# Optimization experiments

Measured on AMD Instinct MI355X. Metric: run time of the kernel, lower is better.

Reference implementation:

```python
import jax, jax.numpy as jnp
from jax import lax
import numpy as np


def _lap(cost):
    """Jonker-Volgenant shortest-augmenting-path LAP (same optimum as
    scipy.optimize.linear_sum_assignment) on cost [n, m] with n <= m.
    Returns for each row (0..n-1) the assigned column index."""
    n, m = cost.shape
    BIG = jnp.asarray(1e9, cost.dtype)
    a = jnp.pad(cost, ((1, 0), (1, 0)))  # 1-based rows/cols, [n+1, m+1]
    u = jnp.zeros(n + 1, cost.dtype)     # row duals
    v = jnp.zeros(m + 1, cost.dtype)     # col duals
    p = jnp.zeros(m + 1, jnp.int32)      # p[j] = row matched to col j (0 = free)

    def row_step(i, carry):
        u, v, p = carry
        p = p.at[0].set(i)  # virtual col 0 holds the row being inserted
        minv = jnp.full(m + 1, BIG, cost.dtype)
        used = jnp.zeros(m + 1, bool)
        way = jnp.zeros(m + 1, jnp.int32)

        def cond(s):
            u, v, p, way, minv, used, j0 = s
            return p[j0] != 0

        def body(s):
            u, v, p, way, minv, used, j0 = s
            used = used.at[j0].set(True)
            i0 = p[j0]
            cur = a[i0] - u[i0] - v                      # reduced costs, len m+1
            better = (cur < minv) & jnp.logical_not(used)
            minv = jnp.where(better, cur, minv)
            way = jnp.where(better, j0, way)
            masked = jnp.where(used, BIG, minv)
            j1 = jnp.argmin(masked).astype(jnp.int32)
            delta = masked[j1]
            u = u.at[p].add(jnp.where(used, delta, jnp.zeros((), cost.dtype)))
            v = jnp.where(used, v - delta, v)
            minv = jnp.where(used, minv, minv - delta)
            return (u, v, p, way, minv, used, j1)

        u, v, p, way, minv, used, j0 = lax.while_loop(
            cond, body, (u, v, p, way, minv, used, jnp.int32(0)))

        # backtrack the augmenting path
        def cond2(s):
            return s[1] != 0

        def body2(s):
            p, j0 = s
            j1 = way[j0]
            return (p.at[j0].set(p[j1]), j1)

        p, _ = lax.while_loop(cond2, body2, (p, j0))
        return (u, v, p)

    u, v, p = lax.fori_loop(1, n + 1, row_step, (u, v, p))
    # invert: row r (1-based) matched to col j  ->  ans[r-1] = j-1
    cols = jnp.arange(m + 1)
    valid = (p > 0) & (cols > 0)
    idx = jnp.where(valid, p - 1, n)  # invalid entries dumped into scratch slot n
    ans = jnp.zeros(n + 1, jnp.int32).at[idx].set((cols - 1).astype(jnp.int32))
    return ans[:n]


def _cdist_mm(x, y):
    """Batched euclidean cdist via the GEMM trick (torch use_mm_for_euclid_dist)."""
    x2 = jnp.sum(x * x, axis=-1)[..., :, None]   # [B, N, 1]
    y2 = jnp.sum(y * y, axis=-1)[..., None, :]   # [B, 1, M]
    xy = jnp.einsum('bnd,bmd->bnm', x, y)        # [B, N, M]
    return jnp.sqrt(jnp.maximum(x2 + y2 - 2.0 * xy, 0.0))


def setup_inputs() -> dict:
    key = jax.random.key(0)
    k1, k2 = jax.random.split(key)
    outputs = jax.random.normal(k1, (32, 512, 768), dtype=jnp.float32)
    targets = jax.random.normal(k2, (32, 200, 768), dtype=jnp.float32)
    return {"outputs": outputs, "targets": targets}


def reference(outputs, targets):
    # cost[b, n, m] = ||outputs[b, n] - targets[b, m]||_2  (block-diagonal slices
    # of the original cross-batch cdist are all that the matcher consumes)
    cost = _cdist_mm(outputs, targets)                       # [B, N, M]
    # solve with targets as rows (n=M <= m=N): pred column per gt row
    gt_to_pred = jax.vmap(_lap)(jnp.swapaxes(cost, 1, 2))    # [B, M]
    # scipy returns pred indices sorted ascending; replicate that ordering
    order = jnp.argsort(gt_to_pred, axis=1)                  # gt indices (index_j)
    index_i = jnp.take_along_axis(gt_to_pred, order, axis=1)
    index_j = order.astype(jnp.int32)
    return jnp.stack([index_i, index_j], axis=1)             # [B, 2, M] int32
```

## Files before the change

kernel.cpp:

```cpp
#include <hip/hip_runtime.h>
#include <math.h>

static constexpr int BATCH = 32;
static constexpr int NPRED = 512;
static constexpr int NTGT  = 200;
static constexpr int DIM   = 768;
#define BIGF  1e9f
#define USEDC 2e9f

__global__ __launch_bounds__(64) void row_norms_kernel(const float* __restrict__ x,
                                                       float* __restrict__ out) {
    int row = blockIdx.x;
    const float4* r = (const float4*)(x + (size_t)row * DIM);
    float s = 0.f;
#pragma unroll
    for (int k = 0; k < 3; ++k) {
        float4 v = r[threadIdx.x + 64 * k];
        s += v.x * v.x + v.y * v.y + v.z * v.z + v.w * v.w;
    }
#pragma unroll
    for (int off = 32; off; off >>= 1) s += __shfl_down(s, off);
    if (threadIdx.x == 0) out[row] = s;
}

__global__ __launch_bounds__(256) void cost_kernel(const float* __restrict__ O,
                                                   const float* __restrict__ T,
                                                   const float* __restrict__ no_arr,
                                                   const float* __restrict__ nt_arr,
                                                   float* __restrict__ cost) {
    const int b  = blockIdx.z;
    const int m0 = blockIdx.y * 32;
    const int n0 = blockIdx.x * 128;
    const float* Tb = T + (size_t)b * NTGT * DIM;
    const float* Ob = O + (size_t)b * NPRED * DIM;

    __shared__ float As[32][33];
    __shared__ float Bs[32][129];

    const int tid = threadIdx.x;
    const int tx = tid & 31;
    const int ty = tid >> 5;

    float acc[4][4] = {};

    for (int k0 = 0; k0 < DIM; k0 += 32) {
        {
            int ar = tid >> 3;
            int ak = (tid & 7) << 2;
            int gm = m0 + ar; if (gm > NTGT - 1) gm = NTGT - 1;
            float4 vA = *(const float4*)(Tb + (size_t)gm * DIM + k0 + ak);
            As[ak + 0][ar] = vA.x; As[ak + 1][ar] = vA.y;
            As[ak + 2][ar] = vA.z; As[ak + 3][ar] = vA.w;
        }
#pragma unroll
        for (int q = 0; q < 4; ++q) {
            int idx = q * 256 + tid;
            int br = idx >> 3;
            int bk = (idx & 7) << 2;
            float4 vB = *(const float4*)(Ob + (size_t)(n0 + br) * DIM + k0 + bk);
            Bs[bk + 0][br] = vB.x; Bs[bk + 1][br] = vB.y;
            Bs[bk + 2][br] = vB.z; Bs[bk + 3][br] = vB.w;
        }
        __syncthreads();
#pragma unroll
        for (int k = 0; k < 32; ++k) {
            float a0 = As[k][ty], a1 = As[k][ty + 8],
                  a2 = As[k][ty + 16], a3 = As[k][ty + 24];
            float b0 = Bs[k][tx],      b1 = Bs[k][tx + 32],
                  b2 = Bs[k][tx + 64], b3 = Bs[k][tx + 96];
            acc[0][0] += a0 * b0; acc[0][1] += a0 * b1; acc[0][2] += a0 * b2; acc[0][3] += a0 * b3;
            acc[1][0] += a1 * b0; acc[1][1] += a1 * b1; acc[1][2] += a1 * b2; acc[1][3] += a1 * b3;
            acc[2][0] += a2 * b0; acc[2][1] += a2 * b1; acc[2][2] += a2 * b2; acc[2][3] += a2 * b3;
            acc[3][0] += a3 * b0; acc[3][1] += a3 * b1; acc[3][2] += a3 * b2; acc[3][3] += a3 * b3;
        }
        __syncthreads();
    }

#pragma unroll
    for (int i = 0; i < 4; ++i) {
        int gm = m0 + ty + 8 * i;
        if (gm < NTGT) {
            float ntv = nt_arr[b * NTGT + gm];
#pragma unroll
            for (int j = 0; j < 4; ++j) {
                int gn = n0 + tx + 32 * j;
                float d2 = ntv + no_arr[b * NPRED + gn] - 2.0f * acc[i][j];
                cost[((size_t)b * NTGT + gm) * NPRED + gn] = sqrtf(fmaxf(d2, 0.0f));
            }
        }
    }
}

__device__ __forceinline__ int rl(int v, int l) {
    return __builtin_amdgcn_readlane(v, l);
}
__device__ __forceinline__ float rlf(float v, int l) {
    return __int_as_float(__builtin_amdgcn_readlane(__float_as_int(v), l));
}
__device__ __forceinline__ int sel8i(const int* a, int s) {
    int r = a[0];
#pragma unroll
    for (int k = 1; k < 8; ++k) r = (s == k) ? a[k] : r;
    return r;
}
__device__ __forceinline__ float sel8f(const float* a, int s) {
    float r = a[0];
#pragma unroll
    for (int k = 1; k < 8; ++k) r = (s == k) ? a[k] : r;
    return r;
}
__device__ __forceinline__ float dpp_min_f32(float x) {
    float t;
    t = __int_as_float(__builtin_amdgcn_update_dpp(__float_as_int(x), __float_as_int(x), 0x111, 0xF, 0xF, false)); x = fminf(x, t);
    t = __int_as_float(__builtin_amdgcn_update_dpp(__float_as_int(x), __float_as_int(x), 0x112, 0xF, 0xF, false)); x = fminf(x, t);
    t = __int_as_float(__builtin_amdgcn_update_dpp(__float_as_int(x), __float_as_int(x), 0x114, 0xF, 0xF, false)); x = fminf(x, t);
    t = __int_as_float(__builtin_amdgcn_update_dpp(__float_as_int(x), __float_as_int(x), 0x118, 0xF, 0xF, false)); x = fminf(x, t);
    t = __int_as_float(__builtin_amdgcn_update_dpp(__float_as_int(x), __float_as_int(x), 0x142, 0xF, 0xF, false)); x = fminf(x, t);
    t = __int_as_float(__builtin_amdgcn_update_dpp(__float_as_int(x), __float_as_int(x), 0x143, 0xF, 0xF, false)); x = fminf(x, t);
    return x;
}
__device__ __forceinline__ float tree8(const float* m, int& lq) {
    float v01 = (m[0] <= m[1]) ? m[0] : m[1];
    int   q01 = (m[0] <= m[1]) ? 0 : 1;
    float v23 = (m[2] <= m[3]) ? m[2] : m[3];
    int   q23 = (m[2] <= m[3]) ? 2 : 3;
    float v45 = (m[4] <= m[5]) ? m[4] : m[5];
    int   q45 = (m[4] <= m[5]) ? 4 : 5;
    float v67 = (m[6] <= m[7]) ? m[6] : m[7];
    int   q67 = (m[6] <= m[7]) ? 6 : 7;
    float v03 = (v01 <= v23) ? v01 : v23;
    int   q03 = (v01 <= v23) ? q01 : q23;
    float v47 = (v45 <= v67) ? v45 : v67;
    int   q47 = (v45 <= v67) ? q45 : q67;
    lq = (v03 <= v47) ? q03 : q47;
    return (v03 <= v47) ? v03 : v47;
}

__global__ __launch_bounds__(64) void lap_kernel(const float* __restrict__ cost,
                                                 int* __restrict__ out) {
    const int b = blockIdx.x;
    const int lane = threadIdx.x;
    const float* C = cost + (size_t)b * NTGT * NPRED;
    const float* Cl = C + lane * 8;

    __shared__ float u0[NTGT + 1];
    __shared__ int g2p[NTGT];

    for (int k = lane; k < NTGT + 1; k += 64) u0[k] = 0.f;

    float v[8], minv[8], up[8];
    int p_arr[8], way_arr[8];
#pragma unroll
    for (int q = 0; q < 8; ++q) {
        v[q] = 0.f; up[q] = 0.f; p_arr[q] = 0; way_arr[q] = 0;
    }
    __syncthreads();

    float4 ca = *(const float4*)(Cl);
    float4 cb = *(const float4*)(Cl + 4);
    float4 sa = ca, sb = cb;

    for (int i = 1; i <= NTGT; ++i) {
#pragma unroll
        for (int q = 0; q < 8; ++q) minv[q] = BIGF;
        float uI = 0.f;
        float u_i0 = 0.f;
        int j0 = 0;
        int j1 = 0;
        int spec_j = 0;

        for (int it = 0; it <= NPRED; ++it) {
            float c[8];
            c[0] = ca.x; c[1] = ca.y; c[2] = ca.z; c[3] = ca.w;
            c[4] = cb.x; c[5] = cb.y; c[6] = cb.z; c[7] = cb.w;

#pragma unroll
            for (int q = 0; q < 8; ++q) {
                float cur = (c[q] - u_i0) - v[q];
                bool usedq = (minv[q] == USEDC);
                float cure = usedq ? USEDC : cur;
                bool imp = cure < minv[q];
                minv[q] = imp ? cure : minv[q];
                way_arr[q] = imp ? j0 : way_arr[q];
            }

            int lq;
            float lval = tree8(minv, lq);
            int   psel = sel8i(p_arr, lq);
            float usel = sel8f(up, lq);
            float wmin = rlf(dpp_min_f32(lval), 63);
            unsigned long long mask = __ballot(lval == wmin);
            int w = (int)__builtin_ctzll(mask);
            int qw  = rl(lq, w);
            int i0n = rl(psel, w);
            float u_n = rlf(usel, w);
            float delta = wmin;
            j1 = w * 8 + qw + 1;
            bool done = (i0n == 0);

            if (!done) {
                if (j1 == spec_j) {
                    ca = sa; cb = sb;
                } else {
                    const float* Crow = Cl + (size_t)(i0n - 1) * NPRED;
                    ca = *(const float4*)(Crow);
                    cb = *(const float4*)(Crow + 4);
                }
            }

            uI += delta;
#pragma unroll
            for (int q = 0; q < 8; ++q) {
                bool usedq = (minv[q] == USEDC);
                v[q]    = usedq ? (v[q] - delta) : v[q];
                up[q]   = usedq ? (up[q] + delta) : up[q];
                minv[q] = usedq ? minv[q] : (minv[q] - delta);
            }
            int j1m1 = j1 - 1;
#pragma unroll
            for (int q = 0; q < 8; ++q) {
                bool mine = (lane * 8 + q) == j1m1;
                minv[q] = mine ? USEDC : minv[q];
            }

            if (done) break;

            {
                int lq2;
                float l2 = tree8(minv, lq2);
                int psel2 = sel8i(p_arr, lq2);
                float w2v = rlf(dpp_min_f32(l2), 63);
                unsigned long long m2 = __ballot(l2 == w2v);
                int w2 = (int)__builtin_ctzll(m2);
                int q2 = rl(lq2, w2);
                int p2 = rl(psel2, w2);
                int spec_new = w2 * 8 + q2 + 1;
                if (p2 != 0 && spec_new != spec_j) {
                    const float* Srow = Cl + (size_t)(p2 - 1) * NPRED;
                    sa = *(const float4*)(Srow);
                    sb = *(const float4*)(Srow + 4);
                }
                spec_j = spec_new;
            }

            u_i0 = u_n;
            j0 = j1;
        }

        if (i < NTGT) {
            const float* Crow = Cl + (size_t)i * NPRED;
            ca = *(const float4*)(Crow);
            cb = *(const float4*)(Crow + 4);
        }

#pragma unroll
        for (int q = 0; q < 8; ++q) {
            bool usedq = (minv[q] == USEDC);
            if (usedq && p_arr[q] != 0) u0[p_arr[q]] = up[q];
        }
        if (lane == 0) u0[i] = uI;

        {
            int j = j1;
            for (int s = 0; s <= NPRED; ++s) {
                int ow = (j - 1) >> 3, oq = (j - 1) & 7;
                int wj = rl(sel8i(way_arr, oq), ow);
                int pOfW;
                if (wj == 0) {
                    pOfW = i;
                } else {
                    int ow2 = (wj - 1) >> 3, oq2 = (wj - 1) & 7;
                    pOfW = rl(sel8i(p_arr, oq2), ow2);
                }
#pragma unroll
                for (int q = 0; q < 8; ++q) {
                    bool mine = (lane == ow) && (q == oq);
                    p_arr[q] = mine ? pOfW : p_arr[q];
                }
                if (wj == 0) break;
                j = wj;
            }
        }

        __syncthreads();
#pragma unroll
        for (int q = 0; q < 8; ++q) up[q] = u0[p_arr[q]];
    }

#pragma unroll
    for (int q = 0; q < 8; ++q) {
        int r = p_arr[q];
        if (r > 0) g2p[r - 1] = lane * 8 + q;
    }
    __syncthreads();

    for (int t = lane; t < NTGT; t += 64) {
        int myv = g2p[t];
        int rank = 0;
        for (int l = 0; l < NTGT; ++l) rank += (g2p[l] < myv) ? 1 : 0;
        out[b * 2 * NTGT + rank] = myv;
        out[b * 2 * NTGT + NTGT + rank] = t;
    }
}

extern "C" void kernel_launch(void* const* d_in, const int* in_sizes, int n_in,
                              void* d_out, int out_size, void* d_ws, size_t ws_size,
                              hipStream_t stream) {
    const float* outputs = (const float*)d_in[0];
    const float* targets = (const float*)d_in[1];
    int* out = (int*)d_out;

    float* cost   = (float*)d_ws;
    float* no_arr = cost + (size_t)BATCH * NTGT * NPRED;
    float* nt_arr = no_arr + (size_t)BATCH * NPRED;

    row_norms_kernel<<<BATCH * NPRED, 64, 0, stream>>>(outputs, no_arr);
    row_norms_kernel<<<BATCH * NTGT, 64, 0, stream>>>(targets, nt_arr);
    cost_kernel<<<dim3(NPRED / 128, (NTGT + 31) / 32, BATCH), 256, 0, stream>>>(
        outputs, targets, no_arr, nt_arr, cost);
    lap_kernel<<<BATCH, 64, 0, stream>>>(cost, out);
}
```

Measured before the change: 879.6 us.

## Fuse cost GEMM and LAP solver with per-tile flags and simplify speculation

Merges the cost-matrix kernel and the LAP solver into one launch. Cost blocks publish completion per (batch, row-tile) through atomic flags, and LAP blocks spin-wait only for the tile they need next, so solving can start before the whole cost matrix exists. The inner loop is also reworked: the used sentinel becomes infinity, and the second-best speculative prefetch candidate now comes from the existing per-lane minima instead of a second tree reduction. LAP blocks now launch with 256 threads but only 64 lanes do useful work. The spin-wait depends on cost blocks being scheduled ahead of the LAP blocks, and the shortcut speculation may pick a less accurate prefetch row.

```diff
diff --git a/kernel.cpp b/kernel.cpp
--- a/kernel.cpp
+++ b/kernel.cpp
@@ -5,8 +5,11 @@
 static constexpr int NPRED = 512;
 static constexpr int NTGT  = 200;
 static constexpr int DIM   = 768;
-#define BIGF  1e9f
-#define USEDC 2e9f
+static constexpr int MTILES = 7;
+static constexpr int NTILES = 4;
+static constexpr int COST_BLOCKS = MTILES * NTILES * BATCH;
+#define BIGF 1e9f
+#define INFF __builtin_inff()
 
 __global__ __launch_bounds__(64) void row_norms_kernel(const float* __restrict__ x,
                                                        float* __restrict__ out) {
@@ -21,74 +24,6 @@
 #pragma unroll
     for (int off = 32; off; off >>= 1) s += __shfl_down(s, off);
     if (threadIdx.x == 0) out[row] = s;
-}
-
-__global__ __launch_bounds__(256) void cost_kernel(const float* __restrict__ O,
-                                                   const float* __restrict__ T,
-                                                   const float* __restrict__ no_arr,
-                                                   const float* __restrict__ nt_arr,
-                                                   float* __restrict__ cost) {
-    const int b  = blockIdx.z;
-    const int m0 = blockIdx.y * 32;
-    const int n0 = blockIdx.x * 128;
-    const float* Tb = T + (size_t)b * NTGT * DIM;
-    const float* Ob = O + (size_t)b * NPRED * DIM;
-
-    __shared__ float As[32][33];
-    __shared__ float Bs[32][129];
-
-    const int tid = threadIdx.x;
-    const int tx = tid & 31;
-    const int ty = tid >> 5;
-
-    float acc[4][4] = {};
-
-    for (int k0 = 0; k0 < DIM; k0 += 32) {
-        {
-            int ar = tid >> 3;
-            int ak = (tid & 7) << 2;
-            int gm = m0 + ar; if (gm > NTGT - 1) gm = NTGT - 1;
-            float4 vA = *(const float4*)(Tb + (size_t)gm * DIM + k0 + ak);
-            As[ak + 0][ar] = vA.x; As[ak + 1][ar] = vA.y;
-            As[ak + 2][ar] = vA.z; As[ak + 3][ar] = vA.w;
-        }
-#pragma unroll
-        for (int q = 0; q < 4; ++q) {
-            int idx = q * 256 + tid;
-            int br = idx >> 3;
-            int bk = (idx & 7) << 2;
-            float4 vB = *(const float4*)(Ob + (size_t)(n0 + br) * DIM + k0 + bk);
-            Bs[bk + 0][br] = vB.x; Bs[bk + 1][br] = vB.y;
-            Bs[bk + 2][br] = vB.z; Bs[bk + 3][br] = vB.w;
-        }
-        __syncthreads();
-#pragma unroll
-        for (int k = 0; k < 32; ++k) {
-            float a0 = As[k][ty], a1 = As[k][ty + 8],
-                  a2 = As[k][ty + 16], a3 = As[k][ty + 24];
-            float b0 = Bs[k][tx],      b1 = Bs[k][tx + 32],
-                  b2 = Bs[k][tx + 64], b3 = Bs[k][tx + 96];
-            acc[0][0] += a0 * b0; acc[0][1] += a0 * b1; acc[0][2] += a0 * b2; acc[0][3] += a0 * b3;
-            acc[1][0] += a1 * b0; acc[1][1] += a1 * b1; acc[1][2] += a1 * b2; acc[1][3] += a1 * b3;
-            acc[2][0] += a2 * b0; acc[2][1] += a2 * b1; acc[2][2] += a2 * b2; acc[2][3] += a2 * b3;
-            acc[3][0] += a3 * b0; acc[3][1] += a3 * b1; acc[3][2] += a3 * b2; acc[3][3] += a3 * b3;
-        }
-        __syncthreads();
-    }
-
-#pragma unroll
-    for (int i = 0; i < 4; ++i) {
-        int gm = m0 + ty + 8 * i;
-        if (gm < NTGT) {
-            float ntv = nt_arr[b * NTGT + gm];
-#pragma unroll
-            for (int j = 0; j < 4; ++j) {
-                int gn = n0 + tx + 32 * j;
-                float d2 = ntv + no_arr[b * NPRED + gn] - 2.0f * acc[i][j];
-                cost[((size_t)b * NTGT + gm) * NPRED + gn] = sqrtf(fmaxf(d2, 0.0f));
-            }
-        }
-    }
 }
 
 __device__ __forceinline__ int rl(int v, int l) {
@@ -136,17 +71,96 @@
     return (v03 <= v47) ? v03 : v47;
 }
 
-__global__ __launch_bounds__(64) void lap_kernel(const float* __restrict__ cost,
-                                                 int* __restrict__ out) {
-    const int b = blockIdx.x;
-    const int lane = threadIdx.x;
+__global__ __launch_bounds__(256) void fused_kernel(const float* __restrict__ O,
+                                                    const float* __restrict__ T,
+                                                    const float* __restrict__ no_arr,
+                                                    const float* __restrict__ nt_arr,
+                                                    float* __restrict__ cost,
+                                                    int* __restrict__ flags,
+                                                    int* __restrict__ out) {
+    if (blockIdx.x < COST_BLOCKS) {
+        const int fb  = blockIdx.x;
+        const int mt  = fb >> 7;
+        const int rm  = fb & 127;
+        const int b   = rm >> 2;
+        const int m0  = mt * 32;
+        const int n0  = (rm & 3) * 128;
+        const float* Tb = T + (size_t)b * NTGT * DIM;
+        const float* Ob = O + (size_t)b * NPRED * DIM;
+
+        __shared__ float As[32][33];
+        __shared__ float Bs[32][129];
+
+        const int tid = threadIdx.x;
+        const int tx = tid & 31;
+        const int ty = tid >> 5;
+
+        float acc[4][4] = {};
+
+        for (int k0 = 0; k0 < DIM; k0 += 32) {
+            {
+                int ar = tid >> 3;
+                int ak = (tid & 7) << 2;
+                int gm = m0 + ar; if (gm > NTGT - 1) gm = NTGT - 1;
+                float4 vA = *(const float4*)(Tb + (size_t)gm * DIM + k0 + ak);
+                As[ak + 0][ar] = vA.x; As[ak + 1][ar] = vA.y;
+                As[ak + 2][ar] = vA.z; As[ak + 3][ar] = vA.w;
+            }
+#pragma unroll
+            for (int q = 0; q < 4; ++q) {
+                int idx = q * 256 + tid;
+                int br = idx >> 3;
+                int bk = (idx & 7) << 2;
+                float4 vB = *(const float4*)(Ob + (size_t)(n0 + br) * DIM + k0 + bk);
+                Bs[bk + 0][br] = vB.x; Bs[bk + 1][br] = vB.y;
+                Bs[bk + 2][br] = vB.z; Bs[bk + 3][br] = vB.w;
+            }
+            __syncthreads();
+#pragma unroll
+            for (int k = 0; k < 32; ++k) {
+                float a0 = As[k][ty], a1 = As[k][ty + 8],
+                      a2 = As[k][ty + 16], a3 = As[k][ty + 24];
+                float b0 = Bs[k][tx],      b1 = Bs[k][tx + 32],
+                      b2 = Bs[k][tx + 64], b3 = Bs[k][tx + 96];
+                acc[0][0] += a0 * b0; acc[0][1] += a0 * b1; acc[0][2] += a0 * b2; acc[0][3] += a0 * b3;
+                acc[1][0] += a1 * b0; acc[1][1] += a1 * b1; acc[1][2] += a1 * b2; acc[1][3] += a1 * b3;
+                acc[2][0] += a2 * b0; acc[2][1] += a2 * b1; acc[2][2] += a2 * b2; acc[2][3] += a2 * b3;
+                acc[3][0] += a3 * b0; acc[3][1] += a3 * b1; acc[3][2] += a3 * b2; acc[3][3] += a3 * b3;
+            }
+            __syncthreads();
+        }
+
+#pragma unroll
+        for (int i = 0; i < 4; ++i) {
+            int gm = m0 + ty + 8 * i;
+            if (gm < NTGT) {
+                float ntv = nt_arr[b * NTGT + gm];
+#pragma unroll
+                for (int j = 0; j < 4; ++j) {
+                    int gn = n0 + tx + 32 * j;
+                    float d2 = ntv + no_arr[b * NPRED + gn] - 2.0f * acc[i][j];
+                    cost[((size_t)b * NTGT + gm) * NPRED + gn] = sqrtf(fmaxf(d2, 0.0f));
+                }
+            }
+        }
+
+        __threadfence();
+        __syncthreads();
+        if (tid == 0)
+            __hip_atomic_fetch_add(&flags[b * MTILES + mt], 1,
+                                   __ATOMIC_RELEASE, __HIP_MEMORY_SCOPE_AGENT);
+        return;
+    }
+
+    const int b = blockIdx.x - COST_BLOCKS;
+    const int lane = threadIdx.x & 63;
     const float* C = cost + (size_t)b * NTGT * NPRED;
     const float* Cl = C + lane * 8;
 
     __shared__ float u0[NTGT + 1];
     __shared__ int g2p[NTGT];
 
-    for (int k = lane; k < NTGT + 1; k += 64) u0[k] = 0.f;
+    for (int k = threadIdx.x; k < NTGT + 1; k += 256) u0[k] = 0.f;
 
     float v[8], minv[8], up[8];
     int p_arr[8], way_arr[8];
@@ -156,6 +170,17 @@
     }
     __syncthreads();
 
+    int waited = -1;
+    auto wait_tile = [&](int t) {
+        if (t > waited) {
+            while (__hip_atomic_load(&flags[b * MTILES + t],
+                                     __ATOMIC_ACQUIRE, __HIP_MEMORY_SCOPE_AGENT) < NTILES)
+                __builtin_amdgcn_s_sleep(16);
+            waited = t;
+        }
+    };
+
+    wait_tile(0);
     float4 ca = *(const float4*)(Cl);
     float4 cb = *(const float4*)(Cl + 4);
     float4 sa = ca, sb = cb;
@@ -174,11 +199,12 @@
             c[0] = ca.x; c[1] = ca.y; c[2] = ca.z; c[3] = ca.w;
             c[4] = cb.x; c[5] = cb.y; c[6] = cb.z; c[7] = cb.w;
 
+            bool used_b[8];
 #pragma unroll
             for (int q = 0; q < 8; ++q) {
                 float cur = (c[q] - u_i0) - v[q];
-                bool usedq = (minv[q] == USEDC);
-                float cure = usedq ? USEDC : cur;
+                used_b[q] = (minv[q] == INFF);
+                float cure = used_b[q] ? INFF : cur;
                 bool imp = cure < minv[q];
                 minv[q] = imp ? cure : minv[q];
                 way_arr[q] = imp ? j0 : way_arr[q];
@@ -206,48 +232,43 @@
                     ca = *(const float4*)(Crow);
                     cb = *(const float4*)(Crow + 4);
                 }
-            }
-
-            uI += delta;
-#pragma unroll
-            for (int q = 0; q < 8; ++q) {
-                bool usedq = (minv[q] == USEDC);
-                v[q]    = usedq ? (v[q] - delta) : v[q];
-                up[q]   = usedq ? (up[q] + delta) : up[q];
-                minv[q] = usedq ? minv[q] : (minv[q] - delta);
-            }
-            int j1m1 = j1 - 1;
-#pragma unroll
-            for (int q = 0; q < 8; ++q) {
-                bool mine = (lane * 8 + q) == j1m1;
-                minv[q] = mine ? USEDC : minv[q];
-            }
-
-            if (done) break;
-
-            {
-                int lq2;
-                float l2 = tree8(minv, lq2);
-                int psel2 = sel8i(p_arr, lq2);
-                float w2v = rlf(dpp_min_f32(l2), 63);
-                unsigned long long m2 = __ballot(l2 == w2v);
+                float lv2 = (lane == w) ? INFF : lval;
+                float wm2 = rlf(dpp_min_f32(lv2), 63);
+                unsigned long long m2 = __ballot(lv2 == wm2);
                 int w2 = (int)__builtin_ctzll(m2);
-                int q2 = rl(lq2, w2);
-                int p2 = rl(psel2, w2);
-                int spec_new = w2 * 8 + q2 + 1;
-                if (p2 != 0 && spec_new != spec_j) {
+                int q2 = rl(lq, w2);
+                int p2 = rl(psel, w2);
+                int sj = w2 * 8 + q2 + 1;
+                if (p2 != 0 && sj != spec_j) {
                     const float* Srow = Cl + (size_t)(p2 - 1) * NPRED;
                     sa = *(const float4*)(Srow);
                     sb = *(const float4*)(Srow + 4);
                 }
-                spec_j = spec_new;
-            }
-
+                spec_j = sj;
+            }
+
+            uI += delta;
+#pragma unroll
+            for (int q = 0; q < 8; ++q) {
+                float d0 = used_b[q] ? delta : 0.f;
+                v[q]  -= d0;
+                up[q] += d0;
+                minv[q] -= delta;
+            }
+            {
+                bool lw = (lane == w);
+#pragma unroll
+                for (int q = 0; q < 8; ++q)
+                    minv[q] = (lw && q == qw) ? INFF : minv[q];
+            }
+
+            if (done) break;
             u_i0 = u_n;
             j0 = j1;
         }
 
         if (i < NTGT) {
+            wait_tile(i >> 5);
             const float* Crow = Cl + (size_t)i * NPRED;
             ca = *(const float4*)(Crow);
             cb = *(const float4*)(Crow + 4);
@@ -255,7 +276,7 @@
 
 #pragma unroll
         for (int q = 0; q < 8; ++q) {
-            bool usedq = (minv[q] == USEDC);
+            bool usedq = (minv[q] == INFF);
             if (usedq && p_arr[q] != 0) u0[p_arr[q]] = up[q];
         }
         if (lane == 0) u0[i] = uI;
@@ -313,10 +334,11 @@
     float* cost   = (float*)d_ws;
     float* no_arr = cost + (size_t)BATCH * NTGT * NPRED;
     float* nt_arr = no_arr + (size_t)BATCH * NPRED;
-
+    int*   flags  = (int*)(nt_arr + (size_t)BATCH * NTGT);
+
+    hipMemsetAsync(flags, 0, BATCH * MTILES * sizeof(int), stream);
     row_norms_kernel<<<BATCH * NPRED, 64, 0, stream>>>(outputs, no_arr);
     row_norms_kernel<<<BATCH * NTGT, 64, 0, stream>>>(targets, nt_arr);
-    cost_kernel<<<dim3(NPRED / 128, (NTGT + 31) / 32, BATCH), 256, 0, stream>>>(
-        outputs, targets, no_arr, nt_arr, cost);
-    lap_kernel<<<BATCH, 64, 0, stream>>>(cost, out);
-}
+    fused_kernel<<<COST_BLOCKS + BATCH, 256, 0, stream>>>(
+        outputs, targets, no_arr, nt_arr, cost, flags, out);
+}
```

New measurement: 1.054 ms. +19.8%, slower.

## Interleave two LAP instances per wavefront to hide serial latency

Applied to the files above, without the earlier changes.

Each 64-lane block now runs the shortest-augmenting-path solvers for two batches, alternating iterations between them. The aim is to hide the latency of each solver's dependent cost-row load and cross-lane reduction behind the other solver's work. The speculative prefetch of the next row is removed, and used columns are now marked with infinity, which makes the dual update uniform. The trade-off is half as many blocks, more register pressure, and no prefetch, so each step now waits on a load that used to be overlapped.

```diff
diff --git a/kernel.cpp b/kernel.cpp
--- a/kernel.cpp
+++ b/kernel.cpp
@@ -5,8 +5,8 @@
 static constexpr int NPRED = 512;
 static constexpr int NTGT  = 200;
 static constexpr int DIM   = 768;
-#define BIGF  1e9f
-#define USEDC 2e9f
+#define BIGF 1e9f
+#define INFF __builtin_inff()
 
 __global__ __launch_bounds__(64) void row_norms_kernel(const float* __restrict__ x,
                                                        float* __restrict__ out) {
@@ -136,58 +136,63 @@
     return (v03 <= v47) ? v03 : v47;
 }
 
-__global__ __launch_bounds__(64) void lap_kernel(const float* __restrict__ cost,
-                                                 int* __restrict__ out) {
-    const int b = blockIdx.x;
+__global__ __launch_bounds__(64) void lap2_kernel(const float* __restrict__ cost,
+                                                  int* __restrict__ out) {
     const int lane = threadIdx.x;
-    const float* C = cost + (size_t)b * NTGT * NPRED;
-    const float* Cl = C + lane * 8;
-
-    __shared__ float u0[NTGT + 1];
-    __shared__ int g2p[NTGT];
-
-    for (int k = lane; k < NTGT + 1; k += 64) u0[k] = 0.f;
-
-    float v[8], minv[8], up[8];
-    int p_arr[8], way_arr[8];
-#pragma unroll
-    for (int q = 0; q < 8; ++q) {
-        v[q] = 0.f; up[q] = 0.f; p_arr[q] = 0; way_arr[q] = 0;
-    }
-    __syncthreads();
-
-    float4 ca = *(const float4*)(Cl);
-    float4 cb = *(const float4*)(Cl + 4);
-    float4 sa = ca, sb = cb;
-
-    for (int i = 1; i <= NTGT; ++i) {
-#pragma unroll
-        for (int q = 0; q < 8; ++q) minv[q] = BIGF;
-        float uI = 0.f;
-        float u_i0 = 0.f;
-        int j0 = 0;
-        int j1 = 0;
-        int spec_j = 0;
-
-        for (int it = 0; it <= NPRED; ++it) {
+    const int b0 = blockIdx.x * 2;
+
+    __shared__ float u0[2][NTGT + 1];
+    __shared__ int g2p[2][NTGT];
+
+    for (int k = lane; k < NTGT + 1; k += 64) { u0[0][k] = 0.f; u0[1][k] = 0.f; }
+
+    const float* Cl_[2] = {
+        cost + (size_t)(b0 + 0) * NTGT * NPRED + lane * 8,
+        cost + (size_t)(b0 + 1) * NTGT * NPRED + lane * 8
+    };
+
+    float v_[2][8], minv_[2][8], up_[2][8];
+    int p_[2][8], way_[2][8];
+    float4 ca[2], cb[2];
+    int ii[2] = {1, 1}, j0_[2] = {0, 0};
+    float ui0_[2] = {0.f, 0.f}, uI_[2] = {0.f, 0.f};
+    bool fin[2] = {false, false};
+
+#pragma unroll
+    for (int k = 0; k < 2; ++k) {
+#pragma unroll
+        for (int q = 0; q < 8; ++q) {
+            v_[k][q] = 0.f; minv_[k][q] = BIGF; up_[k][q] = 0.f;
+            p_[k][q] = 0; way_[k][q] = 0;
+        }
+        ca[k] = *(const float4*)(Cl_[k]);
+        cb[k] = *(const float4*)(Cl_[k] + 4);
+    }
+
+    while (!(fin[0] && fin[1])) {
+#pragma unroll
+        for (int k = 0; k < 2; ++k) {
+            if (fin[k]) continue;
+
             float c[8];
-            c[0] = ca.x; c[1] = ca.y; c[2] = ca.z; c[3] = ca.w;
-            c[4] = cb.x; c[5] = cb.y; c[6] = cb.z; c[7] = cb.w;
-
+            c[0] = ca[k].x; c[1] = ca[k].y; c[2] = ca[k].z; c[3] = ca[k].w;
+            c[4] = cb[k].x; c[5] = cb[k].y; c[6] = cb[k].z; c[7] = cb[k].w;
+
+            bool used_b[8];
 #pragma unroll
             for (int q = 0; q < 8; ++q) {
-                float cur = (c[q] - u_i0) - v[q];
-                bool usedq = (minv[q] == USEDC);
-                float cure = usedq ? USEDC : cur;
-                bool imp = cure < minv[q];
-                minv[q] = imp ? cure : minv[q];
-                way_arr[q] = imp ? j0 : way_arr[q];
+                float cur = (c[q] - ui0_[k]) - v_[k][q];
+                used_b[q] = (minv_[k][q] == INFF);
+                float cure = used_b[q] ? INFF : cur;
+                bool imp = cure < minv_[k][q];
+                minv_[k][q] = imp ? cure : minv_[k][q];
+                way_[k][q] = imp ? j0_[k] : way_[k][q];
             }
 
             int lq;
-            float lval = tree8(minv, lq);
-            int   psel = sel8i(p_arr, lq);
-            float usel = sel8f(up, lq);
+            float lval = tree8(minv_[k], lq);
+            int   psel = sel8i(p_[k], lq);
+            float usel = sel8f(up_[k], lq);
             float wmin = rlf(dpp_min_f32(lval), 63);
             unsigned long long mask = __ballot(lval == wmin);
             int w = (int)__builtin_ctzll(mask);
@@ -195,111 +200,94 @@
             int i0n = rl(psel, w);
             float u_n = rlf(usel, w);
             float delta = wmin;
-            j1 = w * 8 + qw + 1;
+            int j1 = w * 8 + qw + 1;
             bool done = (i0n == 0);
 
             if (!done) {
-                if (j1 == spec_j) {
-                    ca = sa; cb = sb;
-                } else {
-                    const float* Crow = Cl + (size_t)(i0n - 1) * NPRED;
-                    ca = *(const float4*)(Crow);
-                    cb = *(const float4*)(Crow + 4);
+                const float* Crow = Cl_[k] + (size_t)(i0n - 1) * NPRED;
+                ca[k] = *(const float4*)(Crow);
+                cb[k] = *(const float4*)(Crow + 4);
+            }
+
+            uI_[k] += delta;
+#pragma unroll
+            for (int q = 0; q < 8; ++q) {
+                float d0 = used_b[q] ? delta : 0.f;
+                v_[k][q]  -= d0;
+                up_[k][q] += d0;
+                minv_[k][q] -= delta;
+            }
+            {
+                bool lw = (lane == w);
+#pragma unroll
+                for (int q = 0; q < 8; ++q)
+                    minv_[k][q] = (lw && q == qw) ? INFF : minv_[k][q];
+            }
+
+            if (!done) {
+                ui0_[k] = u_n;
+                j0_[k] = j1;
+                continue;
+            }
+
+            int i = ii[k];
+#pragma unroll
+            for (int q = 0; q < 8; ++q) {
+                bool usedq = (minv_[k][q] == INFF);
+                if (usedq && p_[k][q] != 0) u0[k][p_[k][q]] = up_[k][q];
+            }
+            if (lane == 0) u0[k][i] = uI_[k];
+
+            {
+                int j = j1;
+                for (int s = 0; s <= NPRED; ++s) {
+                    int ow = (j - 1) >> 3, oq = (j - 1) & 7;
+                    int wj = rl(sel8i(way_[k], oq), ow);
+                    int pOfW;
+                    if (wj == 0) {
+                        pOfW = i;
+                    } else {
+                        int ow2 = (wj - 1) >> 3, oq2 = (wj - 1) & 7;
+                        pOfW = rl(sel8i(p_[k], oq2), ow2);
+                    }
+#pragma unroll
+                    for (int q = 0; q < 8; ++q) {
+                        bool mine = (lane == ow) && (q == oq);
+                        p_[k][q] = mine ? pOfW : p_[k][q];
+                    }
+                    if (wj == 0) break;
+                    j = wj;
                 }
             }
 
-            uI += delta;
-#pragma unroll
-            for (int q = 0; q < 8; ++q) {
-                bool usedq = (minv[q] == USEDC);
-                v[q]    = usedq ? (v[q] - delta) : v[q];
-                up[q]   = usedq ? (up[q] + delta) : up[q];
-                minv[q] = usedq ? minv[q] : (minv[q] - delta);
-            }
-            int j1m1 = j1 - 1;
-#pragma unroll
-            for (int q = 0; q < 8; ++q) {
-                bool mine = (lane * 8 + q) == j1m1;
-                minv[q] = mine ? USEDC : minv[q];
-            }
-
-            if (done) break;
-
-            {
-                int lq2;
-                float l2 = tree8(minv, lq2);
-                int psel2 = sel8i(p_arr, lq2);
-                float w2v = rlf(dpp_min_f32(l2), 63);
-                unsigned long long m2 = __ballot(l2 == w2v);
-                int w2 = (int)__builtin_ctzll(m2);
-                int q2 = rl(lq2, w2);
-                int p2 = rl(psel2, w2);
-                int spec_new = w2 * 8 + q2 + 1;
-                if (p2 != 0 && spec_new != spec_j) {
-                    const float* Srow = Cl + (size_t)(p2 - 1) * NPRED;
-                    sa = *(const float4*)(Srow);
-                    sb = *(const float4*)(Srow + 4);
+#pragma unroll
+            for (int q = 0; q < 8; ++q) up_[k][q] = u0[k][p_[k][q]];
+
+            ii[k] = i + 1;
+            if (i + 1 > NTGT) {
+                int bb = b0 + k;
+#pragma unroll
+                for (int q = 0; q < 8; ++q) {
+                    int r = p_[k][q];
+                    if (r > 0) g2p[k][r - 1] = lane * 8 + q;
                 }
-                spec_j = spec_new;
-            }
-
-            u_i0 = u_n;
-            j0 = j1;
-        }
-
-        if (i < NTGT) {
-            const float* Crow = Cl + (size_t)i * NPRED;
-            ca = *(const float4*)(Crow);
-            cb = *(const float4*)(Crow + 4);
-        }
-
-#pragma unroll
-        for (int q = 0; q < 8; ++q) {
-            bool usedq = (minv[q] == USEDC);
-            if (usedq && p_arr[q] != 0) u0[p_arr[q]] = up[q];
-        }
-        if (lane == 0) u0[i] = uI;
-
-        {
-            int j = j1;
-            for (int s = 0; s <= NPRED; ++s) {
-                int ow = (j - 1) >> 3, oq = (j - 1) & 7;
-                int wj = rl(sel8i(way_arr, oq), ow);
-                int pOfW;
-                if (wj == 0) {
-                    pOfW = i;
-                } else {
-                    int ow2 = (wj - 1) >> 3, oq2 = (wj - 1) & 7;
-                    pOfW = rl(sel8i(p_arr, oq2), ow2);
+                for (int t = lane; t < NTGT; t += 64) {
+                    int myv = g2p[k][t];
+                    int rank = 0;
+                    for (int l = 0; l < NTGT; ++l) rank += (g2p[k][l] < myv) ? 1 : 0;
+                    out[bb * 2 * NTGT + rank] = myv;
+                    out[bb * 2 * NTGT + NTGT + rank] = t;
                 }
-#pragma unroll
-                for (int q = 0; q < 8; ++q) {
-                    bool mine = (lane == ow) && (q == oq);
-                    p_arr[q] = mine ? pOfW : p_arr[q];
-                }
-                if (wj == 0) break;
-                j = wj;
-            }
-        }
-
-        __syncthreads();
-#pragma unroll
-        for (int q = 0; q < 8; ++q) up[q] = u0[p_arr[q]];
-    }
-
-#pragma unroll
-    for (int q = 0; q < 8; ++q) {
-        int r = p_arr[q];
-        if (r > 0) g2p[r - 1] = lane * 8 + q;
-    }
-    __syncthreads();
-
-    for (int t = lane; t < NTGT; t += 64) {
-        int myv = g2p[t];
-        int rank = 0;
-        for (int l = 0; l < NTGT; ++l) rank += (g2p[l] < myv) ? 1 : 0;
-        out[b * 2 * NTGT + rank] = myv;
-        out[b * 2 * NTGT + NTGT + rank] = t;
+                fin[k] = true;
+            } else {
+#pragma unroll
+                for (int q = 0; q < 8; ++q) minv_[k][q] = BIGF;
+                uI_[k] = 0.f; ui0_[k] = 0.f; j0_[k] = 0;
+                const float* Crow = Cl_[k] + (size_t)i * NPRED;
+                ca[k] = *(const float4*)(Crow);
+                cb[k] = *(const float4*)(Crow + 4);
+            }
+        }
     }
 }
 
@@ -318,5 +306,5 @@
     row_norms_kernel<<<BATCH * NTGT, 64, 0, stream>>>(targets, nt_arr);
     cost_kernel<<<dim3(NPRED / 128, (NTGT + 31) / 32, BATCH), 256, 0, stream>>>(
         outputs, targets, no_arr, nt_arr, cost);
-    lap_kernel<<<BATCH, 64, 0, stream>>>(cost, out);
-}
+    lap2_kernel<<<BATCH / 2, 64, 0, stream>>>(cost, out);
+}
```

Result: slower. 1.381 ms (+57.0%).
